# Kernel tuning notes

Measured on AMD Instinct MI355X. Metric: run time of the kernel, lower is better.

Reference implementation:

```python
import jax, jax.numpy as jnp
import numpy as np

B, L, D = 4096, 50, 64
NU, NI, NR = 100000, 100000, 5


def setup_inputs() -> dict:
    key = jax.random.key(0)
    ks = jax.random.split(key, 16)
    s = 0.02
    inp = {
        "nodes_v": jax.random.randint(ks[0], (B,), 0, NI),
        "neigh_u": jax.random.randint(ks[1], (B, L), 0, NU),
        "neigh_r": jax.random.randint(ks[2], (B, L), 0, NR),
        "embed_u": jax.random.normal(ks[3], (NU, D)) * s,
        "embed_i": jax.random.normal(ks[4], (NI, D)) * s,
        "embed_r": jax.random.normal(ks[5], (NR, D)) * s,
        # gv MLP: Linear(2D,D) ReLU Linear(D,D) ReLU Linear(D,D)
        "gv_w1": jax.random.normal(ks[6], (2 * D, D)) * s, "gv_b1": jnp.zeros((D,)),
        "gv_w2": jax.random.normal(ks[7], (D, D)) * s,     "gv_b2": jnp.zeros((D,)),
        "gv_w3": jax.random.normal(ks[8], (D, D)) * s,     "gv_b3": jnp.zeros((D,)),
        # attention MLP: Linear(2D,D) ReLU Linear(D,D) ReLU Linear(D,1), softmax over neighbors
        "att_w1": jax.random.normal(ks[9], (2 * D, D)) * s, "att_b1": jnp.zeros((D,)),
        "att_w2": jax.random.normal(ks[10], (D, D)) * s,    "att_b2": jnp.zeros((D,)),
        "att_w3": jax.random.normal(ks[11], (D, 1)) * s,    "att_b3": jnp.zeros((1,)),
        # combine: Linear(2D,D) ReLU Linear(D,D) ReLU
        "wr1_w": jax.random.normal(ks[12], (2 * D, D)) * s, "wr1_b": jnp.zeros((D,)),
        "wr2_w": jax.random.normal(ks[13], (D, D)) * s,     "wr2_b": jnp.zeros((D,)),
    }
    return inp


def reference(nodes_v, neigh_u, neigh_r, embed_u, embed_i, embed_r,
              gv_w1, gv_b1, gv_w2, gv_b2, gv_w3, gv_b3,
              att_w1, att_b1, att_w2, att_b2, att_w3, att_b3,
              wr1_w, wr1_b, wr2_w, wr2_b):
    qj = embed_i[nodes_v]            # [B, D] item reps
    pt = embed_u[neigh_u]            # [B, L, D] neighbor user reps
    er = embed_r[neigh_r]            # [B, L, D] rating reps
    # fusion MLP g(.)
    x = jnp.concatenate([pt, er], axis=-1)                    # [B, L, 2D]
    h = jax.nn.relu(x @ gv_w1 + gv_b1)
    h = jax.nn.relu(h @ gv_w2 + gv_b2)
    fjt = h @ gv_w3 + gv_b3                                   # [B, L, D]
    # attention over neighbors (dropout is identity in eval mode)
    q_rep = jnp.broadcast_to(qj[:, None, :], fjt.shape)       # [B, L, D]
    a = jnp.concatenate([fjt, q_rep], axis=-1)                # [B, L, 2D]
    a = jax.nn.relu(a @ att_w1 + att_b1)
    a = jax.nn.relu(a @ att_w2 + att_b2)
    scores = (a @ att_w3 + att_b3)[..., 0]                    # [B, L]
    mu = jax.nn.softmax(scores, axis=1)                       # softmax over neighbors
    zj = jnp.einsum("bld,bl->bd", fjt, mu)                   # weighted aggregation
    # combine aggregated neighborhood with item's own embedding (2D -> D)
    z = jax.nn.relu(jnp.concatenate([zj, qj], axis=-1) @ wr1_w + wr1_b)
    out = jax.nn.relu(z @ wr2_w + wr2_b)                      # [B, D]
    return out
```

## Files before the change

kernel.cpp:

```cpp
#include <hip/hip_runtime.h>

typedef __bf16 bf16;
typedef short s16x8 __attribute__((ext_vector_type(8)));
typedef __bf16 b16x8 __attribute__((ext_vector_type(8)));
typedef float f32x4 __attribute__((ext_vector_type(4)));

#define B_   4096
#define L_   50
#define SH   72

#define OFF_W1F  0
#define OFF_W2F  8192
#define OFF_W3F  12288
#define OFF_WCF  16384
#define OFF_A2F  20480
#define OFF_R1T  24576
#define OFF_R2T  32768
#define WT_TOTAL 36864
#define BIAS1P_BYTE 73728
#define CQ_BYTE     73984

#define PREP_W_BLOCKS 145
#define PREP_C_BLOCKS 1024

__device__ __forceinline__ unsigned short f2b(float f) {
    __bf16 h = (__bf16)f;
    return __builtin_bit_cast(unsigned short, h);
}
__device__ __forceinline__ unsigned pack2(float a, float b) {
    return (unsigned)f2b(a) | ((unsigned)f2b(b) << 16);
}
__device__ __forceinline__ s16x8 mkfrag(float4 a, float4 b) {
    union { s16x8 v; unsigned u[4]; } r;
    r.u[0] = pack2(a.x, a.y); r.u[1] = pack2(a.z, a.w);
    r.u[2] = pack2(b.x, b.y); r.u[3] = pack2(b.z, b.w);
    return r.v;
}
__device__ __forceinline__ f32x4 mfma16(s16x8 a, s16x8 b, f32x4 c) {
    return __builtin_amdgcn_mfma_f32_16x16x32_bf16(a, b, c, 0, 0, 0);
}

extern "C" __global__ void prep_all(const float* __restrict__ w1, const float* __restrict__ w2,
                                    const float* __restrict__ w3, const float* __restrict__ a1,
                                    const float* __restrict__ a2, const float* __restrict__ r1,
                                    const float* __restrict__ r2, const float* __restrict__ gb3,
                                    const float* __restrict__ ab1,
                                    const int* __restrict__ nodes_v, const float* __restrict__ embed_i,
                                    bf16* __restrict__ wt, float* __restrict__ bias1p,
                                    float* __restrict__ cq)
{
    if (blockIdx.x >= PREP_W_BLOCKS) {
        int gid = (blockIdx.x - PREP_W_BLOCKS) * 256 + threadIdx.x;
        int b = gid >> 6, n = gid & 63;
        int v = nodes_v[b];
        const float* q = embed_i + v * 64;
        float s0 = 0.f, s1 = 0.f, s2 = 0.f, s3 = 0.f;
#pragma unroll
        for (int k = 0; k < 64; k += 4) {
            s0 = fmaf(q[k],     a1[(64 + k) * 64 + n],     s0);
            s1 = fmaf(q[k + 1], a1[(64 + k + 1) * 64 + n], s1);
            s2 = fmaf(q[k + 2], a1[(64 + k + 2) * 64 + n], s2);
            s3 = fmaf(q[k + 3], a1[(64 + k + 3) * 64 + n], s3);
        }
        cq[gid] = (s0 + s1) + (s2 + s3);
        return;
    }
    int i = blockIdx.x * 256 + threadIdx.x;
    if (i >= WT_TOTAL + 64) return;
    if (i >= WT_TOTAL) {
        int n = i - WT_TOTAL;
        float s0 = ab1[n], s1 = 0.f, s2 = 0.f, s3 = 0.f;
#pragma unroll
        for (int t = 0; t < 64; t += 4) {
            s0 = fmaf(gb3[t],     a1[t * 64 + n],       s0);
            s1 = fmaf(gb3[t + 1], a1[(t + 1) * 64 + n], s1);
            s2 = fmaf(gb3[t + 2], a1[(t + 2) * 64 + n], s2);
            s3 = fmaf(gb3[t + 3], a1[(t + 3) * 64 + n], s3);
        }
        bias1p[n] = (s0 + s1) + (s2 + s3);
        return;
    }
    float val;
    if (i < OFF_R1T) {
        int off, kind;
        if      (i < OFF_W2F) { off = OFF_W1F; kind = 0; }
        else if (i < OFF_W3F) { off = OFF_W2F; kind = 1; }
        else if (i < OFF_WCF) { off = OFF_W3F; kind = 2; }
        else if (i < OFF_A2F) { off = OFF_WCF; kind = 3; }
        else                  { off = OFF_A2F; kind = 4; }
        int local = i - off;
        int f = local >> 9, lane = (local >> 3) & 63, j = local & 7;
        int kt = f >> 2, nt = f & 3, quad = lane >> 4, m = lane & 15;
        int k = kt * 32 + quad * 8 + j;
        int n = nt * 16 + m;
        if (kind == 0)      val = w1[k * 64 + n];
        else if (kind == 1) val = w2[k * 64 + n];
        else if (kind == 2) val = w3[k * 64 + n];
        else if (kind == 4) val = a2[k * 64 + n];
        else {
            float s0 = 0.f, s1 = 0.f, s2 = 0.f, s3 = 0.f;
#pragma unroll
            for (int t = 0; t < 64; t += 4) {
                float4 w = *(const float4*)(w3 + k * 64 + t);
                s0 = fmaf(w.x, a1[t * 64 + n],       s0);
                s1 = fmaf(w.y, a1[(t + 1) * 64 + n], s1);
                s2 = fmaf(w.z, a1[(t + 2) * 64 + n], s2);
                s3 = fmaf(w.w, a1[(t + 3) * 64 + n], s3);
            }
            val = (s0 + s1) + (s2 + s3);
        }
    }
    else if (i < OFF_R2T) { int li = i - OFF_R1T; int n = li >> 7, k = li & 127; val = r1[k * 64 + n]; }
    else                  { int li = i - OFF_R2T; int n = li >> 6, k = li & 63;  val = r2[k * 64 + n]; }
    wt[i] = (bf16)val;
}

extern "C" __global__ void __launch_bounds__(256, 2)
dense_fused(const int* __restrict__ nodes_v, const int* __restrict__ neigh_u,
            const int* __restrict__ neigh_r,
            const float* __restrict__ embed_u, const float* __restrict__ embed_i,
            const float* __restrict__ embed_r,
            const float* __restrict__ gv_b1, const float* __restrict__ gv_b2,
            const float* __restrict__ gv_b3,
            const float* __restrict__ att_b2, const float* __restrict__ att_w3,
            const float* __restrict__ wr1_b, const float* __restrict__ wr2_b,
            const bf16* __restrict__ wt, const float* __restrict__ cq,
            const float* __restrict__ bias1p, float* __restrict__ out)
{
    __shared__ __align__(16) bf16 H[128 * SH];
    __shared__ float zp[4 * 64];
    __shared__ float swm[4 * 2];
    __shared__ float qsh[2 * 64];

    const int tid = threadIdx.x;
    const int lane = tid & 63, wave = tid >> 6;
    const int m = lane & 15, quad = lane >> 4;
    const int b0 = blockIdx.x * 2;
    const int rw0 = wave * 32;
    const int item_w = rw0 >> 6;
    const int lbase = rw0 & 63;

    const int bw = b0 + item_w;
    const int l0 = min(lbase + m, L_ - 1);
    const int l1 = min(lbase + 16 + m, L_ - 1);
    const int u0 = neigh_u[bw * L_ + l0], u1 = neigh_u[bw * L_ + l1];
    const int v0 = neigh_r[bw * L_ + l0], v1 = neigh_r[bw * L_ + l1];

    float cs4[4];
#pragma unroll
    for (int nt = 0; nt < 4; ++nt) {
        int c = nt * 16 + m;
        cs4[nt] = cq[bw * 64 + c] + bias1p[c];
    }

    bf16* Hw = H + rw0 * SH;
    bf16* H0 = Hw;
    bf16* H1 = Hw + 16 * SH;

    {
        const float* b00 = embed_u + u0 * 64;
        const float* b01 = embed_u + u1 * 64;
        const float* b10 = embed_r + v0 * 64;
        const float* b11 = embed_r + v1 * 64;
        f32x4 ac0[4] = {}, ac1[4] = {};
#pragma unroll
        for (int kt = 0; kt < 4; ++kt) {
            const float* s0p = (kt < 2 ? b00 : b10) + (kt & 1) * 32 + quad * 8;
            const float* s1p = (kt < 2 ? b01 : b11) + (kt & 1) * 32 + quad * 8;
            float4 a0a = *(const float4*)s0p, a0b = *(const float4*)(s0p + 4);
            float4 a1a = *(const float4*)s1p, a1b = *(const float4*)(s1p + 4);
            s16x8 a0 = mkfrag(a0a, a0b);
            s16x8 a1 = mkfrag(a1a, a1b);
#pragma unroll
            for (int nt = 0; nt < 4; ++nt) {
                s16x8 b = *(const s16x8*)(wt + OFF_W1F + (kt * 4 + nt) * 512 + lane * 8);
                ac0[nt] = mfma16(a0, b, ac0[nt]);
                ac1[nt] = mfma16(a1, b, ac1[nt]);
            }
        }
#pragma unroll
        for (int nt = 0; nt < 4; ++nt) {
            int c = nt * 16 + m;
            float bv = gv_b1[c];
#pragma unroll
            for (int r4 = 0; r4 < 4; ++r4) {
                H0[(quad * 4 + r4) * SH + c] = (bf16)fmaxf(ac0[nt][r4] + bv, 0.f);
                H1[(quad * 4 + r4) * SH + c] = (bf16)fmaxf(ac1[nt][r4] + bv, 0.f);
            }
        }
    }

    {
        f32x4 ac0[4] = {}, ac1[4] = {};
#pragma unroll
        for (int kt = 0; kt < 2; ++kt) {
            s16x8 a0 = *(const s16x8*)(H0 + m * SH + kt * 32 + quad * 8);
            s16x8 a1 = *(const s16x8*)(H1 + m * SH + kt * 32 + quad * 8);
#pragma unroll
            for (int nt = 0; nt < 4; ++nt) {
                s16x8 b = *(const s16x8*)(wt + OFF_W2F + (kt * 4 + nt) * 512 + lane * 8);
                ac0[nt] = mfma16(a0, b, ac0[nt]);
                ac1[nt] = mfma16(a1, b, ac1[nt]);
            }
        }
#pragma unroll
        for (int nt = 0; nt < 4; ++nt) {
            int c = nt * 16 + m;
            float bv = gv_b2[c];
#pragma unroll
            for (int r4 = 0; r4 < 4; ++r4) {
                H0[(quad * 4 + r4) * SH + c] = (bf16)fmaxf(ac0[nt][r4] + bv, 0.f);
                H1[(quad * 4 + r4) * SH + c] = (bf16)fmaxf(ac1[nt][r4] + bv, 0.f);
            }
        }
    }

    f32x4 aF0[4] = {}, aF1[4] = {};
    {
        f32x4 aA0[4] = {}, aA1[4] = {};
#pragma unroll
        for (int kt = 0; kt < 2; ++kt) {
            s16x8 a0 = *(const s16x8*)(H0 + m * SH + kt * 32 + quad * 8);
            s16x8 a1 = *(const s16x8*)(H1 + m * SH + kt * 32 + quad * 8);
#pragma unroll
            for (int nt = 0; nt < 4; ++nt) {
                s16x8 bF = *(const s16x8*)(wt + OFF_W3F + (kt * 4 + nt) * 512 + lane * 8);
                s16x8 bA = *(const s16x8*)(wt + OFF_WCF + (kt * 4 + nt) * 512 + lane * 8);
                aF0[nt] = mfma16(a0, bF, aF0[nt]);
                aF1[nt] = mfma16(a1, bF, aF1[nt]);
                aA0[nt] = mfma16(a0, bA, aA0[nt]);
                aA1[nt] = mfma16(a1, bA, aA1[nt]);
            }
        }
#pragma unroll
        for (int nt = 0; nt < 4; ++nt) {
            int c = nt * 16 + m;
#pragma unroll
            for (int r4 = 0; r4 < 4; ++r4) {
                H0[(quad * 4 + r4) * SH + c] = (bf16)fmaxf(aA0[nt][r4] + cs4[nt], 0.f);
                H1[(quad * 4 + r4) * SH + c] = (bf16)fmaxf(aA1[nt][r4] + cs4[nt], 0.f);
            }
        }
    }

    float s0[4], s1[4];
    {
        f32x4 ac0[4] = {}, ac1[4] = {};
#pragma unroll
        for (int kt = 0; kt < 2; ++kt) {
            s16x8 a0 = *(const s16x8*)(H0 + m * SH + kt * 32 + quad * 8);
            s16x8 a1 = *(const s16x8*)(H1 + m * SH + kt * 32 + quad * 8);
#pragma unroll
            for (int nt = 0; nt < 4; ++nt) {
                s16x8 b = *(const s16x8*)(wt + OFF_A2F + (kt * 4 + nt) * 512 + lane * 8);
                ac0[nt] = mfma16(a0, b, ac0[nt]);
                ac1[nt] = mfma16(a1, b, ac1[nt]);
            }
        }
#pragma unroll
        for (int r4 = 0; r4 < 4; ++r4) { s0[r4] = 0.f; s1[r4] = 0.f; }
#pragma unroll
        for (int nt = 0; nt < 4; ++nt) {
            int c = nt * 16 + m;
            float b2v = att_b2[c], w3v = att_w3[c];
#pragma unroll
            for (int r4 = 0; r4 < 4; ++r4) {
                s0[r4] += fmaxf(ac0[nt][r4] + b2v, 0.f) * w3v;
                s1[r4] += fmaxf(ac1[nt][r4] + b2v, 0.f) * w3v;
            }
        }
#pragma unroll
        for (int mask = 1; mask < 16; mask <<= 1)
#pragma unroll
            for (int r4 = 0; r4 < 4; ++r4) {
                s0[r4] += __shfl_xor(s0[r4], mask);
                s1[r4] += __shfl_xor(s1[r4], mask);
            }
    }

    {
        const int r0b = lbase + quad * 4;
        float mloc = -1e30f;
#pragma unroll
        for (int r4 = 0; r4 < 4; ++r4) {
            if (r0b + r4 < L_)      mloc = fmaxf(mloc, s0[r4]);
            if (r0b + 16 + r4 < L_) mloc = fmaxf(mloc, s1[r4]);
        }
        mloc = fmaxf(mloc, __shfl_xor(mloc, 16));
        mloc = fmaxf(mloc, __shfl_xor(mloc, 32));

        float e0[4], e1[4], ssum = 0.f;
#pragma unroll
        for (int r4 = 0; r4 < 4; ++r4) {
            e0[r4] = (r0b + r4 < L_)      ? __expf(s0[r4] - mloc) : 0.f;
            e1[r4] = (r0b + 16 + r4 < L_) ? __expf(s1[r4] - mloc) : 0.f;
            ssum += e0[r4] + e1[r4];
        }
        ssum += __shfl_xor(ssum, 16);
        ssum += __shfl_xor(ssum, 32);

        float z[4] = {0.f, 0.f, 0.f, 0.f};
#pragma unroll
        for (int r4 = 0; r4 < 4; ++r4)
#pragma unroll
            for (int nt = 0; nt < 4; ++nt)
                z[nt] += aF0[nt][r4] * e0[r4] + aF1[nt][r4] * e1[r4];
#pragma unroll
        for (int nt = 0; nt < 4; ++nt) {
            z[nt] += __shfl_xor(z[nt], 16);
            z[nt] += __shfl_xor(z[nt], 32);
        }
        if (quad == 0) {
#pragma unroll
            for (int nt = 0; nt < 4; ++nt) zp[wave * 64 + nt * 16 + m] = z[nt];
        }
        if (lane == 0) { swm[wave * 2] = ssum; swm[wave * 2 + 1] = mloc; }
    }
    __syncthreads();

    if ((wave & 1) == 0) {
        const int item = wave >> 1;
        const int d = lane;
        float ma = swm[wave * 2 + 1],      mb = swm[(wave + 1) * 2 + 1];
        float sa = swm[wave * 2],          sb = swm[(wave + 1) * 2];
        float M  = fmaxf(ma, mb);
        float fa = __expf(ma - M), fb = __expf(mb - M);
        float zj = (fa * zp[wave * 64 + d] + fb * zp[(wave + 1) * 64 + d])
                 / (fa * sa + fb * sb) + gv_b3[d];

        float* zsh = zp + wave * 64;
        zsh[d] = zj;
        qsh[item * 64 + d] = embed_i[nodes_v[b0 + item] * 64 + d];

        float accz = wr1_b[d];
        const bf16* r1 = wt + OFF_R1T + d * 128;
#pragma unroll
        for (int k8 = 0; k8 < 8; ++k8) {
            b16x8 wv = *(const b16x8*)(r1 + k8 * 8);
#pragma unroll
            for (int j = 0; j < 8; ++j) accz = fmaf((float)wv[j], zsh[k8 * 8 + j], accz);
        }
#pragma unroll
        for (int k8 = 0; k8 < 8; ++k8) {
            b16x8 wv = *(const b16x8*)(r1 + 64 + k8 * 8);
#pragma unroll
            for (int j = 0; j < 8; ++j) accz = fmaf((float)wv[j], qsh[item * 64 + k8 * 8 + j], accz);
        }
        zsh[d] = fmaxf(accz, 0.f);

        float acco = wr2_b[d];
        const bf16* r2 = wt + OFF_R2T + d * 64;
#pragma unroll
        for (int k8 = 0; k8 < 8; ++k8) {
            b16x8 wv = *(const b16x8*)(r2 + k8 * 8);
#pragma unroll
            for (int j = 0; j < 8; ++j) acco = fmaf((float)wv[j], zsh[k8 * 8 + j], acco);
        }
        out[(b0 + item) * 64 + d] = fmaxf(acco, 0.f);
    }
}

extern "C" void kernel_launch(void* const* d_in, const int* in_sizes, int n_in,
                              void* d_out, int out_size, void* d_ws, size_t ws_size,
                              hipStream_t stream)
{
    const int* nodes_v = (const int*)d_in[0];
    const int* neigh_u = (const int*)d_in[1];
    const int* neigh_r = (const int*)d_in[2];
    const float* embed_u = (const float*)d_in[3];
    const float* embed_i = (const float*)d_in[4];
    const float* embed_r = (const float*)d_in[5];
    const float* gv_w1  = (const float*)d_in[6];  const float* gv_b1 = (const float*)d_in[7];
    const float* gv_w2  = (const float*)d_in[8];  const float* gv_b2 = (const float*)d_in[9];
    const float* gv_w3  = (const float*)d_in[10]; const float* gv_b3 = (const float*)d_in[11];
    const float* att_w1 = (const float*)d_in[12]; const float* att_b1 = (const float*)d_in[13];
    const float* att_w2 = (const float*)d_in[14]; const float* att_b2 = (const float*)d_in[15];
    const float* att_w3 = (const float*)d_in[16]; const float* att_b3 = (const float*)d_in[17];
    const float* wr1_w  = (const float*)d_in[18]; const float* wr1_b = (const float*)d_in[19];
    const float* wr2_w  = (const float*)d_in[20]; const float* wr2_b = (const float*)d_in[21];
    (void)att_b3;

    bf16*  wt     = (bf16*)d_ws;
    float* bias1p = (float*)((char*)d_ws + BIAS1P_BYTE);
    float* cq     = (float*)((char*)d_ws + CQ_BYTE);

    prep_all<<<PREP_W_BLOCKS + PREP_C_BLOCKS, 256, 0, stream>>>(
        gv_w1, gv_w2, gv_w3, att_w1, att_w2, wr1_w, wr2_w, gv_b3, att_b1,
        nodes_v, embed_i, wt, bias1p, cq);
    dense_fused<<<B_ / 2, 256, 0, stream>>>(nodes_v, neigh_u, neigh_r,
                                            embed_u, embed_i, embed_r,
                                            gv_b1, gv_b2, gv_b3, att_b2, att_w3,
                                            wr1_b, wr2_b, wt, cq, bias1p, (float*)d_out);
}
```

Before: 168.2 us.

## Pre-convert embedding tables to bf16 and use one item per 128-thread block

Adds a conversion pass inside the prep kernel that rewrites the whole user and rating embedding tables to bf16 in workspace, so the fused kernel gathers half-size rows with no in-kernel conversion. The fused kernel now handles one item per 128-thread block instead of two items per 256-thread block. Converting the full 100000x64 user table reads about 25.6MB and writes 12.8MB on every call, while the gather only touches about 200K rows. That extra whole-table traffic may outweigh the savings on the gather. The bf16 path is chosen only when the workspace is large enough.

Measured after the change: 164.6 us. 2.1% less time.

```diff
diff --git a/kernel.cpp b/kernel.cpp
--- a/kernel.cpp
+++ b/kernel.cpp
@@ -19,9 +19,14 @@
 #define WT_TOTAL 36864
 #define BIAS1P_BYTE 73728
 #define CQ_BYTE     73984
+#define EU16_BYTE   1122560
+#define ER16_BYTE   13922560
+#define WS_NEED     13923200
 
 #define PREP_W_BLOCKS 145
 #define PREP_C_BLOCKS 1024
+#define CONV_THREADS  800040
+#define CONV_BLOCKS   3126
 
 __device__ __forceinline__ unsigned short f2b(float f) {
     __bf16 h = (__bf16)f;
@@ -46,9 +51,25 @@
                                     const float* __restrict__ r2, const float* __restrict__ gb3,
                                     const float* __restrict__ ab1,
                                     const int* __restrict__ nodes_v, const float* __restrict__ embed_i,
+                                    const float* __restrict__ embed_u, const float* __restrict__ embed_r,
                                     bf16* __restrict__ wt, float* __restrict__ bias1p,
-                                    float* __restrict__ cq)
+                                    float* __restrict__ cq,
+                                    bf16* __restrict__ eu16, bf16* __restrict__ er16)
 {
+    if (blockIdx.x >= PREP_W_BLOCKS + PREP_C_BLOCKS) {
+        long t = (long)(blockIdx.x - PREP_W_BLOCKS - PREP_C_BLOCKS) * 256 + threadIdx.x;
+        if (t < 800000) {
+            const float* s = embed_u + t * 8;
+            float4 a = *(const float4*)s, b = *(const float4*)(s + 4);
+            *(s16x8*)(eu16 + t * 8) = mkfrag(a, b);
+        } else if (t < CONV_THREADS) {
+            long r = (t - 800000) * 8;
+            const float* s = embed_r + r;
+            float4 a = *(const float4*)s, b = *(const float4*)(s + 4);
+            *(s16x8*)(er16 + r) = mkfrag(a, b);
+        }
+        return;
+    }
     if (blockIdx.x >= PREP_W_BLOCKS) {
         int gid = (blockIdx.x - PREP_W_BLOCKS) * 256 + threadIdx.x;
         int b = gid >> 6, n = gid & 63;
@@ -115,7 +136,8 @@
     wt[i] = (bf16)val;
 }
 
-extern "C" __global__ void __launch_bounds__(256, 2)
+template<bool BF16E>
+__global__ void __launch_bounds__(128, 4)
 dense_fused(const int* __restrict__ nodes_v, const int* __restrict__ neigh_u,
             const int* __restrict__ neigh_r,
             const float* __restrict__ embed_u, const float* __restrict__ embed_i,
@@ -124,58 +146,75 @@
             const float* __restrict__ gv_b3,
             const float* __restrict__ att_b2, const float* __restrict__ att_w3,
             const float* __restrict__ wr1_b, const float* __restrict__ wr2_b,
-            const bf16* __restrict__ wt, const float* __restrict__ cq,
+            const bf16* __restrict__ wt, const bf16* __restrict__ eu16,
+            const bf16* __restrict__ er16, const float* __restrict__ cq,
             const float* __restrict__ bias1p, float* __restrict__ out)
 {
-    __shared__ __align__(16) bf16 H[128 * SH];
-    __shared__ float zp[4 * 64];
-    __shared__ float swm[4 * 2];
-    __shared__ float qsh[2 * 64];
+    __shared__ __align__(16) bf16 H[64 * SH];
+    __shared__ float zp[2 * 64];
+    __shared__ float swm[2 * 2];
+    __shared__ float qsh[64];
 
     const int tid = threadIdx.x;
     const int lane = tid & 63, wave = tid >> 6;
     const int m = lane & 15, quad = lane >> 4;
-    const int b0 = blockIdx.x * 2;
-    const int rw0 = wave * 32;
-    const int item_w = rw0 >> 6;
-    const int lbase = rw0 & 63;
-
-    const int bw = b0 + item_w;
+    const int b = blockIdx.x;
+    const int lbase = wave * 32;
+
     const int l0 = min(lbase + m, L_ - 1);
     const int l1 = min(lbase + 16 + m, L_ - 1);
-    const int u0 = neigh_u[bw * L_ + l0], u1 = neigh_u[bw * L_ + l1];
-    const int v0 = neigh_r[bw * L_ + l0], v1 = neigh_r[bw * L_ + l1];
+    const int u0 = neigh_u[b * L_ + l0], u1 = neigh_u[b * L_ + l1];
+    const int v0 = neigh_r[b * L_ + l0], v1 = neigh_r[b * L_ + l1];
 
     float cs4[4];
 #pragma unroll
     for (int nt = 0; nt < 4; ++nt) {
         int c = nt * 16 + m;
-        cs4[nt] = cq[bw * 64 + c] + bias1p[c];
-    }
-
-    bf16* Hw = H + rw0 * SH;
-    bf16* H0 = Hw;
-    bf16* H1 = Hw + 16 * SH;
+        cs4[nt] = cq[b * 64 + c] + bias1p[c];
+    }
+
+    bf16* H0 = H + lbase * SH;
+    bf16* H1 = H0 + 16 * SH;
 
     {
-        const float* b00 = embed_u + u0 * 64;
-        const float* b01 = embed_u + u1 * 64;
-        const float* b10 = embed_r + v0 * 64;
-        const float* b11 = embed_r + v1 * 64;
         f32x4 ac0[4] = {}, ac1[4] = {};
-#pragma unroll
-        for (int kt = 0; kt < 4; ++kt) {
-            const float* s0p = (kt < 2 ? b00 : b10) + (kt & 1) * 32 + quad * 8;
-            const float* s1p = (kt < 2 ? b01 : b11) + (kt & 1) * 32 + quad * 8;
-            float4 a0a = *(const float4*)s0p, a0b = *(const float4*)(s0p + 4);
-            float4 a1a = *(const float4*)s1p, a1b = *(const float4*)(s1p + 4);
-            s16x8 a0 = mkfrag(a0a, a0b);
-            s16x8 a1 = mkfrag(a1a, a1b);
-#pragma unroll
-            for (int nt = 0; nt < 4; ++nt) {
-                s16x8 b = *(const s16x8*)(wt + OFF_W1F + (kt * 4 + nt) * 512 + lane * 8);
-                ac0[nt] = mfma16(a0, b, ac0[nt]);
-                ac1[nt] = mfma16(a1, b, ac1[nt]);
+        if constexpr (BF16E) {
+            const bf16* p00 = eu16 + (size_t)u0 * 64;
+            const bf16* p01 = eu16 + (size_t)u1 * 64;
+            const bf16* p10 = er16 + v0 * 64;
+            const bf16* p11 = er16 + v1 * 64;
+#pragma unroll
+            for (int kt = 0; kt < 4; ++kt) {
+                const bf16* s0p = (kt < 2 ? p00 : p10) + (kt & 1) * 32 + quad * 8;
+                const bf16* s1p = (kt < 2 ? p01 : p11) + (kt & 1) * 32 + quad * 8;
+                s16x8 a0 = *(const s16x8*)s0p;
+                s16x8 a1 = *(const s16x8*)s1p;
+#pragma unroll
+                for (int nt = 0; nt < 4; ++nt) {
+                    s16x8 bfr = *(const s16x8*)(wt + OFF_W1F + (kt * 4 + nt) * 512 + lane * 8);
+                    ac0[nt] = mfma16(a0, bfr, ac0[nt]);
+                    ac1[nt] = mfma16(a1, bfr, ac1[nt]);
+                }
+            }
+        } else {
+            const float* b00 = embed_u + (size_t)u0 * 64;
+            const float* b01 = embed_u + (size_t)u1 * 64;
+            const float* b10 = embed_r + v0 * 64;
+            const float* b11 = embed_r + v1 * 64;
+#pragma unroll
+            for (int kt = 0; kt < 4; ++kt) {
+                const float* s0p = (kt < 2 ? b00 : b10) + (kt & 1) * 32 + quad * 8;
+                const float* s1p = (kt < 2 ? b01 : b11) + (kt & 1) * 32 + quad * 8;
+                float4 a0a = *(const float4*)s0p, a0b = *(const float4*)(s0p + 4);
+                float4 a1a = *(const float4*)s1p, a1b = *(const float4*)(s1p + 4);
+                s16x8 a0 = mkfrag(a0a, a0b);
+                s16x8 a1 = mkfrag(a1a, a1b);
+#pragma unroll
+                for (int nt = 0; nt < 4; ++nt) {
+                    s16x8 bfr = *(const s16x8*)(wt + OFF_W1F + (kt * 4 + nt) * 512 + lane * 8);
+                    ac0[nt] = mfma16(a0, bfr, ac0[nt]);
+                    ac1[nt] = mfma16(a1, bfr, ac1[nt]);
+                }
             }
         }
 #pragma unroll
@@ -198,9 +237,9 @@
             s16x8 a1 = *(const s16x8*)(H1 + m * SH + kt * 32 + quad * 8);
 #pragma unroll
             for (int nt = 0; nt < 4; ++nt) {
-                s16x8 b = *(const s16x8*)(wt + OFF_W2F + (kt * 4 + nt) * 512 + lane * 8);
-                ac0[nt] = mfma16(a0, b, ac0[nt]);
-                ac1[nt] = mfma16(a1, b, ac1[nt]);
+                s16x8 bfr = *(const s16x8*)(wt + OFF_W2F + (kt * 4 + nt) * 512 + lane * 8);
+                ac0[nt] = mfma16(a0, bfr, ac0[nt]);
+                ac1[nt] = mfma16(a1, bfr, ac1[nt]);
             }
         }
 #pragma unroll
@@ -252,9 +291,9 @@
             s16x8 a1 = *(const s16x8*)(H1 + m * SH + kt * 32 + quad * 8);
 #pragma unroll
             for (int nt = 0; nt < 4; ++nt) {
-                s16x8 b = *(const s16x8*)(wt + OFF_A2F + (kt * 4 + nt) * 512 + lane * 8);
-                ac0[nt] = mfma16(a0, b, ac0[nt]);
-                ac1[nt] = mfma16(a1, b, ac1[nt]);
+                s16x8 bfr = *(const s16x8*)(wt + OFF_A2F + (kt * 4 + nt) * 512 + lane * 8);
+                ac0[nt] = mfma16(a0, bfr, ac0[nt]);
+                ac1[nt] = mfma16(a1, bfr, ac1[nt]);
             }
         }
 #pragma unroll
@@ -318,19 +357,17 @@
     }
     __syncthreads();
 
-    if ((wave & 1) == 0) {
-        const int item = wave >> 1;
+    if (wave == 0) {
         const int d = lane;
-        float ma = swm[wave * 2 + 1],      mb = swm[(wave + 1) * 2 + 1];
-        float sa = swm[wave * 2],          sb = swm[(wave + 1) * 2];
+        float ma = swm[1], mb = swm[3];
+        float sa = swm[0], sb = swm[2];
         float M  = fmaxf(ma, mb);
         float fa = __expf(ma - M), fb = __expf(mb - M);
-        float zj = (fa * zp[wave * 64 + d] + fb * zp[(wave + 1) * 64 + d])
-                 / (fa * sa + fb * sb) + gv_b3[d];
-
-        float* zsh = zp + wave * 64;
+        float zj = (fa * zp[d] + fb * zp[64 + d]) / (fa * sa + fb * sb) + gv_b3[d];
+
+        float* zsh = zp;
         zsh[d] = zj;
-        qsh[item * 64 + d] = embed_i[nodes_v[b0 + item] * 64 + d];
+        qsh[d] = embed_i[nodes_v[b] * 64 + d];
 
         float accz = wr1_b[d];
         const bf16* r1 = wt + OFF_R1T + d * 128;
@@ -344,7 +381,7 @@
         for (int k8 = 0; k8 < 8; ++k8) {
             b16x8 wv = *(const b16x8*)(r1 + 64 + k8 * 8);
 #pragma unroll
-            for (int j = 0; j < 8; ++j) accz = fmaf((float)wv[j], qsh[item * 64 + k8 * 8 + j], accz);
+            for (int j = 0; j < 8; ++j) accz = fmaf((float)wv[j], qsh[k8 * 8 + j], accz);
         }
         zsh[d] = fmaxf(accz, 0.f);
 
@@ -356,7 +393,7 @@
 #pragma unroll
             for (int j = 0; j < 8; ++j) acco = fmaf((float)wv[j], zsh[k8 * 8 + j], acco);
         }
-        out[(b0 + item) * 64 + d] = fmaxf(acco, 0.f);
+        out[b * 64 + d] = fmaxf(acco, 0.f);
     }
 }
 
@@ -383,12 +420,27 @@
     bf16*  wt     = (bf16*)d_ws;
     float* bias1p = (float*)((char*)d_ws + BIAS1P_BYTE);
     float* cq     = (float*)((char*)d_ws + CQ_BYTE);
-
-    prep_all<<<PREP_W_BLOCKS + PREP_C_BLOCKS, 256, 0, stream>>>(
+    bf16*  eu16   = (bf16*)((char*)d_ws + EU16_BYTE);
+    bf16*  er16   = (bf16*)((char*)d_ws + ER16_BYTE);
+
+    const bool big = ws_size >= (size_t)WS_NEED;
+    const int prep_grid = PREP_W_BLOCKS + PREP_C_BLOCKS + (big ? CONV_BLOCKS : 0);
+
+    prep_all<<<prep_grid, 256, 0, stream>>>(
         gv_w1, gv_w2, gv_w3, att_w1, att_w2, wr1_w, wr2_w, gv_b3, att_b1,
-        nodes_v, embed_i, wt, bias1p, cq);
-    dense_fused<<<B_ / 2, 256, 0, stream>>>(nodes_v, neigh_u, neigh_r,
-                                            embed_u, embed_i, embed_r,
-                                            gv_b1, gv_b2, gv_b3, att_b2, att_w3,
-                                            wr1_b, wr2_b, wt, cq, bias1p, (float*)d_out);
-}
+        nodes_v, embed_i, embed_u, embed_r, wt, bias1p, cq, eu16, er16);
+
+    if (big) {
+        dense_fused<true><<<B_, 128, 0, stream>>>(nodes_v, neigh_u, neigh_r,
+                                                  embed_u, embed_i, embed_r,
+                                                  gv_b1, gv_b2, gv_b3, att_b2, att_w3,
+                                                  wr1_b, wr2_b, wt, eu16, er16,
+                                                  cq, bias1p, (float*)d_out);
+    } else {
+        dense_fused<false><<<B_, 128, 0, stream>>>(nodes_v, neigh_u, neigh_r,
+                                                   embed_u, embed_i, embed_r,
+                                                   gv_b1, gv_b2, gv_b3, att_b2, att_w3,
+                                                   wr1_b, wr2_b, wt, eu16, er16,
+                                                   cq, bias1p, (float*)d_out);
+    }
+}
```
